# Optimization experiments

Hardware: AMD Instinct MI355X
Metric: run time of the kernel (lower is better)

The kernel has to match this reference:

```python
import jax, jax.numpy as jnp
import numpy as np

N_HEADS = 8
HEAD_SIZE = 64
CONTEXT = 256
D_MODEL = 512
MASK_NEG = 1e9


def setup_inputs() -> dict:
    key = jax.random.key(0)
    k1, k2, k3, k4 = jax.random.split(key, 4)
    B, T, D = 2, 4096, D_MODEL
    # Glorot-uniform-ish scales
    def glorot(k, shape):
        fan_in, fan_out = shape[-2], shape[-1]
        lim = jnp.sqrt(6.0 / (fan_in + fan_out))
        return jax.random.uniform(k, shape, jnp.float32, -lim, lim)
    inputs = jax.random.normal(k1, (B, T, D), dtype=jnp.float32)
    WQ = glorot(k2, (N_HEADS, D, HEAD_SIZE))
    WV = glorot(k3, (N_HEADS, D, HEAD_SIZE))
    WU = glorot(k4, (N_HEADS * HEAD_SIZE, D))
    return {"inputs": inputs, "WQ": WQ, "WV": WV, "WU": WU}


def reference(inputs, WQ, WV, WU):
    B, T, D = inputs.shape
    H, _, S = WQ.shape
    # Q, V: [B, H, T, hs]
    Q = jnp.einsum('btd,hds->bhts', inputs, WQ)
    V = jnp.einsum('btd,hds->bhts', inputs, WV)
    # Scores use Q @ V^T (no separate K in this module): [B, H, T, T]
    scores = jnp.einsum('bhts,bhus->bhtu', Q, V) / jnp.sqrt(jnp.float32(S))
    idx = jnp.arange(T)
    band = jnp.abs(idx[:, None] - idx[None, :]) <= CONTEXT  # [T, T] bool
    scores = scores - MASK_NEG * (~band).astype(scores.dtype)
    W = jax.nn.softmax(scores, axis=-1)
    C = jnp.einsum('bhtu,bhus->bhts', W, V)  # [B, H, T, hs]
    # concat heads along feature dim: [B, T, H*hs]
    C = C.transpose(0, 2, 1, 3).reshape(B, T, H * S)
    return C @ WU  # [B, T, D]
```

## Files before the change

kernel.cpp:

```cpp
#include <hip/hip_runtime.h>

#define TSEQ 4096
#define DM 512
#define NH 8
#define HS 64
#define CTX 256

typedef __attribute__((ext_vector_type(8))) short bf16x8;
typedef __attribute__((ext_vector_type(4))) float f32x4;
typedef unsigned short u16;
typedef unsigned long long ull;

__device__ __forceinline__ u16 f2bf(float x) {
    unsigned u = __float_as_uint(x);
    unsigned r = (u + 0x7fffu + ((u >> 16) & 1u)) >> 16;
    return (u16)r;
}
__device__ __forceinline__ float bf2f(u16 b) {
    return __uint_as_float(((unsigned)b) << 16);
}
__device__ __forceinline__ unsigned bf16dup(float p) {
    unsigned w;
    asm("v_cvt_pk_bf16_f32 %0, %1, %1" : "=v"(w) : "v"(p));
    return w;
}
template<int CTRL>
__device__ __forceinline__ float dpp_ror(float x) {
    int xi = __float_as_int(x);
    return __int_as_float(__builtin_amdgcn_update_dpp(xi, xi, CTRL, 0xf, 0xf, false));
}
__device__ __forceinline__ float row16_max(float v) {
    v = fmaxf(v, dpp_ror<0x121>(v));
    v = fmaxf(v, dpp_ror<0x122>(v));
    v = fmaxf(v, dpp_ror<0x124>(v));
    v = fmaxf(v, dpp_ror<0x128>(v));
    return v;
}

#define MFMA(a, b, c) __builtin_amdgcn_mfma_f32_16x16x32_bf16((a), (b), (c), 0, 0, 0)

__global__ __launch_bounds__(256) void presplit_x(
    const float* __restrict__ X, u16* __restrict__ Xh)
{
    size_t idx = ((size_t)blockIdx.x * 256 + threadIdx.x) * 8;
    float4 p0 = *(const float4*)(X + idx);
    float4 p1 = *(const float4*)(X + idx + 4);
    float v[8] = {p0.x, p0.y, p0.z, p0.w, p1.x, p1.y, p1.z, p1.w};
    bf16x8 h;
    #pragma unroll
    for (int i = 0; i < 8; ++i) h[i] = (short)f2bf(v[i]);
    *(bf16x8*)(Xh + idx) = h;
}

__global__ __launch_bounds__(256) void presplit_w(
    const float* __restrict__ WQ, const float* __restrict__ WV,
    const float* __restrict__ WU,
    u16* __restrict__ WQt_h, u16* __restrict__ WVt_h, u16* __restrict__ WUt_h)
{
    int gidx = blockIdx.x * 256 + threadIdx.x;
    int a = gidx >> 18;
    int r = gidx & 262143;
    float val;
    u16* dh;
    int dst;
    if (a < 2) {
        int h = r >> 15, s = (r >> 9) & 63, d = r & 511;
        const float* W = (a == 0) ? WQ : WV;
        val = W[h * 32768 + d * 64 + s];
        dst = h * 32768 + s * 512 + d;
        dh = (a == 0) ? WQt_h : WVt_h;
    } else {
        int n = r >> 9, k = r & 511;
        val = WU[k * 512 + n];
        dst = n * 512 + k;
        dh = WUt_h;
    }
    dh[dst] = f2bf(val);
}

__global__ __launch_bounds__(256) void gemm_mfma(
    const u16* __restrict__ Ah_g,
    const u16* __restrict__ B0h, const u16* __restrict__ B1h,
    u16* __restrict__ O0h,
    u16* __restrict__ O1h,
    u16* __restrict__ O1t,
    float* __restrict__ Of,
    int mode)
{
    __shared__ u16 Ah[128][64];
    __shared__ u16 Bh[64][64];

    const int tid = threadIdx.x;
    const int w = tid >> 6, lane = tid & 63;
    const int lg = lane >> 4, ln = lane & 15;
    const int r0 = blockIdx.x * 128;
    const int y = blockIdx.y;

    const u16* Bsh;
    if (mode == 0) {
        Bsh = ((y < 8) ? B0h + (size_t)y * 32768 : B1h + (size_t)(y - 8) * 32768);
    } else {
        Bsh = B0h + (size_t)y * 64 * 512;
    }

    const int r_a = tid >> 3;
    const int kc  = tid & 7;
    const int wcol = (kc * 8) ^ ((r_a & 7) << 3);
    const size_t gA = (size_t)(r0 + r_a) * DM + kc * 8;
    const size_t gB = (size_t)r_a * 512 + kc * 8;

    bf16x8 a0h, a1h, a2h, a3h, b0h, b1h;

    #define GLOAD(k0)                                                   \
        a0h = *(const bf16x8*)(Ah_g + gA + (k0));                       \
        a1h = *(const bf16x8*)(Ah_g + gA + 32 * DM + (k0));             \
        a2h = *(const bf16x8*)(Ah_g + gA + 64 * DM + (k0));             \
        a3h = *(const bf16x8*)(Ah_g + gA + 96 * DM + (k0));             \
        b0h = *(const bf16x8*)(Bsh + gB + (k0));                        \
        b1h = *(const bf16x8*)(Bsh + gB + 32 * 512 + (k0));

    f32x4 acc[2][4];
    #pragma unroll
    for (int i = 0; i < 2; ++i)
        #pragma unroll
        for (int j = 0; j < 4; ++j)
            acc[i][j] = (f32x4){0.f, 0.f, 0.f, 0.f};

    GLOAD(0);

    for (int kt = 0; kt < 8; ++kt) {
        __syncthreads();
        *(bf16x8*)&Ah[r_a][wcol]      = a0h;
        *(bf16x8*)&Ah[r_a + 32][wcol] = a1h;
        *(bf16x8*)&Ah[r_a + 64][wcol] = a2h;
        *(bf16x8*)&Ah[r_a + 96][wcol] = a3h;
        *(bf16x8*)&Bh[r_a][wcol]      = b0h;
        *(bf16x8*)&Bh[r_a + 32][wcol] = b1h;
        __syncthreads();
        if (kt < 7) { GLOAD((kt + 1) * 64); }

        #pragma unroll
        for (int kk = 0; kk < 2; ++kk) {
            const int fc = (kk * 32 + lg * 8) ^ ((ln & 7) << 3);
            bf16x8 ah[2], bh2[4];
            #pragma unroll
            for (int ti = 0; ti < 2; ++ti)
                ah[ti] = *(const bf16x8*)&Ah[w * 32 + ti * 16 + ln][fc];
            #pragma unroll
            for (int nj = 0; nj < 4; ++nj)
                bh2[nj] = *(const bf16x8*)&Bh[nj * 16 + ln][fc];
            #pragma unroll
            for (int ti = 0; ti < 2; ++ti)
                #pragma unroll
                for (int nj = 0; nj < 4; ++nj)
                    acc[ti][nj] = MFMA(ah[ti], bh2[nj], acc[ti][nj]);
        }
    }
    #undef GLOAD

    const float qscale = (mode == 0 && y < 8) ? 0.18033688f : 1.0f;
    #pragma unroll
    for (int ti = 0; ti < 2; ++ti)
        #pragma unroll
        for (int nj = 0; nj < 4; ++nj) {
            u16 hb[4];
            #pragma unroll
            for (int r = 0; r < 4; ++r) {
                float val = acc[ti][nj][r] * qscale;
                hb[r] = f2bf(val);
                int t = r0 + w * 32 + ti * 16 + lg * 4 + r;
                int n = nj * 16 + ln;
                if (mode == 0) {
                    int bh = (t >> 12) * NH + (y & 7);
                    size_t off = ((size_t)bh * TSEQ + (t & (TSEQ - 1))) * HS + n;
                    if (y < 8) O0h[off] = hb[r];
                    else       O1h[off] = hb[r];
                } else {
                    Of[(size_t)t * DM + y * 64 + n] = val;
                }
            }
            if (mode == 0 && y >= 8) {
                int t = r0 + w * 32 + ti * 16 + lg * 4;
                int n = nj * 16 + ln;
                int bh = (t >> 12) * NH + (y & 7);
                size_t off = (size_t)bh * TSEQ * HS + (size_t)n * TSEQ + (t & (TSEQ - 1));
                ull pk = (ull)hb[0] | ((ull)hb[1] << 16)
                       | ((ull)hb[2] << 32) | ((ull)hb[3] << 48);
                *(ull*)(O1t + off) = pk;
            }
        }
}

__global__ __launch_bounds__(256) void attn_v9(
    const u16* __restrict__ Qh_g,
    const u16* __restrict__ Vnh_g, const u16* __restrict__ Vth_g,
    u16* __restrict__ Ch)
{
    __shared__ u16 Vn_h[64][64];
    __shared__ u16 Vt_h[64][64];
    __shared__ unsigned Ps[4][16][32];

    const int tid = threadIdx.x;
    const int w = tid >> 6, lane = tid & 63;
    const int lg = lane >> 4, ln = lane & 15;
    const int raw = blockIdx.x;
    const int swz = (raw & 7) * 128 + (raw >> 3);
    const int ttile = swz & 63;
    const int bh = swz >> 6;
    const int t0 = ttile * 64;
    const size_t base = (size_t)bh * TSEQ * HS;
    const u16* Qph = Qh_g + base;
    const u16* Vph = Vnh_g + base;
    const u16* Vth = Vth_g + base;

    bf16x8 qh[2];
    #pragma unroll
    for (int kk = 0; kk < 2; ++kk) {
        size_t off = (size_t)(t0 + w * 16 + ln) * HS + kk * 32 + lg * 8;
        qh[kk] = *(const bf16x8*)(Qph + off);
    }

    bf16x8 ones_frag;
    #pragma unroll
    for (int e = 0; e < 8; ++e)
        ones_frag[e] = (ln == 0) ? (short)0x3F80 : (short)0;

    f32x4 o[4], o4;
    float m[4];
    #pragma unroll
    for (int j = 0; j < 4; ++j) {
        o[j] = (f32x4){0.f, 0.f, 0.f, 0.f};
        m[j] = -1e30f;
    }
    o4 = (f32x4){0.f, 0.f, 0.f, 0.f};

    int u_lo = t0 - CTX; if (u_lo < 0) u_lo = 0;
    int u_hi = t0 + 64 + CTX; if (u_hi > TSEQ) u_hi = TSEQ;

    const int sr = tid >> 3;
    const int c8 = (tid & 7) * 8;
    const int wcA = c8 ^ ((sr & 7) << 3);

    bf16x8 vn0h, vn1h, vt0h, vt1h;
    #define VL(u0v)                                                             \
        vn0h = *(const bf16x8*)(Vph + (size_t)((u0v) + sr) * HS + c8);          \
        vn1h = *(const bf16x8*)(Vph + (size_t)((u0v) + sr + 32) * HS + c8);     \
        vt0h = *(const bf16x8*)(Vth + (size_t)sr * TSEQ + (u0v) + c8);          \
        vt1h = *(const bf16x8*)(Vth + (size_t)(sr + 32) * TSEQ + (u0v) + c8);

    VL(u_lo);

    for (int u0 = u_lo; u0 < u_hi; u0 += 64) {
        __syncthreads();
        *(bf16x8*)&Vn_h[sr][wcA]      = vn0h;
        *(bf16x8*)&Vn_h[sr + 32][wcA] = vn1h;
        *(bf16x8*)&Vt_h[sr][wcA]      = vt0h;
        *(bf16x8*)&Vt_h[sr + 32][wcA] = vt1h;
        __syncthreads();
        if (u0 + 64 < u_hi) { VL(u0 + 64); }

        f32x4 s[4];
        #pragma unroll
        for (int j = 0; j < 4; ++j) s[j] = (f32x4){0.f, 0.f, 0.f, 0.f};

        #pragma unroll
        for (int kk = 0; kk < 2; ++kk) {
            const int fc = (kk * 32 + lg * 8) ^ ((ln & 7) << 3);
            bf16x8 vh[4];
            #pragma unroll
            for (int uj = 0; uj < 4; ++uj)
                vh[uj] = *(const bf16x8*)&Vn_h[uj * 16 + ln][fc];
            #pragma unroll
            for (int uj = 0; uj < 4; ++uj)
                s[uj] = MFMA(qh[kk], vh[uj], s[uj]);
        }

        bool needmask = ((t0 + 63 - u0) > CTX) || ((u0 + 63 - t0) > CTX);
        if (needmask) {
            #pragma unroll
            for (int uj = 0; uj < 4; ++uj)
                #pragma unroll
                for (int r = 0; r < 4; ++r) {
                    int t = t0 + w * 16 + lg * 4 + r;
                    int u = u0 + uj * 16 + ln;
                    int d = t - u; if (d < 0) d = -d;
                    if (d > CTX) s[uj][r] = -1e30f;
                }
        }

        float rm[4];
        bool need = false;
        #pragma unroll
        for (int r = 0; r < 4; ++r) {
            float v = fmaxf(fmaxf(s[0][r], s[1][r]), fmaxf(s[2][r], s[3][r]));
            rm[r] = row16_max(v);
            need |= (rm[r] > m[r] + 8.f);
        }
        if (__any(need)) {
            #pragma unroll
            for (int r = 0; r < 4; ++r) {
                float mn = fmaxf(m[r], rm[r]);
                float sc2 = exp2f(m[r] - mn);
                m[r] = mn;
                o4[r] *= sc2;
                #pragma unroll
                for (int sj = 0; sj < 4; ++sj)
                    o[sj][r] *= sc2;
            }
        }
        #pragma unroll
        for (int r = 0; r < 4; ++r)
            #pragma unroll
            for (int uj = 0; uj < 4; ++uj)
                s[uj][r] = exp2f(s[uj][r] - m[r]);

        #pragma unroll
        for (int kk = 0; kk < 2; ++kk) {
            #pragma unroll
            for (int u2 = 0; u2 < 2; ++u2) {
                int uj = kk * 2 + u2;
                #pragma unroll
                for (int r = 0; r < 4; ++r) {
                    int trow = lg * 4 + r;
                    int ucol = (u2 * 16 + ln) ^ ((trow & 7) << 2);
                    Ps[w][trow][ucol] = bf16dup(s[uj][r]);
                }
            }

            bf16x8 ph, vth4[4];
            {
                int sw = (ln & 7) << 2;
                uint4 q0 = *(const uint4*)&Ps[w][ln][(lg * 8) ^ sw];
                uint4 q1 = *(const uint4*)&Ps[w][ln][(lg * 8 + 4) ^ sw];
                union { unsigned u[4]; bf16x8 v; } H;
                H.u[0] = __builtin_amdgcn_perm(q0.y, q0.x, 0x05040100u);
                H.u[1] = __builtin_amdgcn_perm(q0.w, q0.z, 0x05040100u);
                H.u[2] = __builtin_amdgcn_perm(q1.y, q1.x, 0x05040100u);
                H.u[3] = __builtin_amdgcn_perm(q1.w, q1.z, 0x05040100u);
                ph = H.v;
            }
            const int fct = (kk * 32 + lg * 8) ^ ((ln & 7) << 3);
            #pragma unroll
            for (int sj = 0; sj < 4; ++sj)
                vth4[sj] = *(const bf16x8*)&Vt_h[sj * 16 + ln][fct];
            #pragma unroll
            for (int sj = 0; sj < 4; ++sj)
                o[sj] = MFMA(ph, vth4[sj], o[sj]);
            o4 = MFMA(ph, ones_frag, o4);
        }
    }
    #undef VL

    const int b = bh >> 3, h = bh & 7;
    #pragma unroll
    for (int r = 0; r < 4; ++r) {
        float ls = __shfl(o4[r], (lane >> 4) << 4);
        float inv = 1.f / ls;
        int t = t0 + w * 16 + lg * 4 + r;
        #pragma unroll
        for (int sj = 0; sj < 4; ++sj) {
            int ss = sj * 16 + ln;
            float val = o[sj][r] * inv;
            size_t off = ((size_t)(b * TSEQ + t)) * DM + h * HS + ss;
            Ch[off] = f2bf(val);
        }
    }
}

extern "C" void kernel_launch(void* const* d_in, const int* in_sizes, int n_in,
                              void* d_out, int out_size, void* d_ws, size_t ws_size,
                              hipStream_t stream) {
    const float* X  = (const float*)d_in[0];
    const float* WQ = (const float*)d_in[1];
    const float* WV = (const float*)d_in[2];
    const float* WU = (const float*)d_in[3];
    float* out = (float*)d_out;

    const size_t SZ = 8388608;
    char* ws = (char*)d_ws;

    u16* Xh = (u16*)(ws);
    u16* Qh = (u16*)(ws + 2 * SZ);
    u16* Vh = (u16*)(ws + 4 * SZ);
    u16* Vth = (u16*)(ws + 6 * SZ);
    char* wsw = ws + 8 * SZ;
    u16* WQt_h = (u16*)(wsw);
    u16* WVt_h = (u16*)(wsw + 524288);
    u16* WUt_h = (u16*)(wsw + 2 * 524288);

    presplit_x<<<2048, 256, 0, stream>>>(X, Xh);
    presplit_w<<<3072, 256, 0, stream>>>(WQ, WV, WU, WQt_h, WVt_h, WUt_h);
    gemm_mfma<<<dim3(64, 16), 256, 0, stream>>>(
        Xh, WQt_h, WVt_h, Qh, Vh, Vth, nullptr, 0);
    attn_v9<<<1024, 256, 0, stream>>>(Qh, Vh, Vth, Xh);
    gemm_mfma<<<dim3(64, 8), 256, 0, stream>>>(
        Xh, WUt_h, nullptr, nullptr, nullptr, nullptr, out, 1);
}
```

Measured before the change: 78.22 us.

## Process 128-key chunks in attention and split output GEMM into smaller tiles

The attention kernel now stages 128 keys per shared-memory load instead of 64 and processes two 64-key halves per barrier pair, which cuts synchronisation and load-loop overhead. The output projection gets a dedicated kernel with 64-row tiles and twice as many blocks, for better occupancy of the GPU. The cost is more shared memory and registers per attention block, which may lower occupancy.

```diff
diff --git a/kernel.cpp b/kernel.cpp
--- a/kernel.cpp
+++ b/kernel.cpp
@@ -78,14 +78,12 @@
     dh[dst] = f2bf(val);
 }
 
-__global__ __launch_bounds__(256) void gemm_mfma(
+__global__ __launch_bounds__(256) void gemm_qv(
     const u16* __restrict__ Ah_g,
     const u16* __restrict__ B0h, const u16* __restrict__ B1h,
     u16* __restrict__ O0h,
     u16* __restrict__ O1h,
-    u16* __restrict__ O1t,
-    float* __restrict__ Of,
-    int mode)
+    u16* __restrict__ O1t)
 {
     __shared__ u16 Ah[128][64];
     __shared__ u16 Bh[64][64];
@@ -96,12 +94,8 @@
     const int r0 = blockIdx.x * 128;
     const int y = blockIdx.y;
 
-    const u16* Bsh;
-    if (mode == 0) {
-        Bsh = ((y < 8) ? B0h + (size_t)y * 32768 : B1h + (size_t)(y - 8) * 32768);
-    } else {
-        Bsh = B0h + (size_t)y * 64 * 512;
-    }
+    const u16* Bsh = (y < 8) ? B0h + (size_t)y * 32768
+                             : B1h + (size_t)(y - 8) * 32768;
 
     const int r_a = tid >> 3;
     const int kc  = tid & 7;
@@ -158,7 +152,7 @@
     }
     #undef GLOAD
 
-    const float qscale = (mode == 0 && y < 8) ? 0.18033688f : 1.0f;
+    const float qscale = (y < 8) ? 0.18033688f : 1.0f;
     #pragma unroll
     for (int ti = 0; ti < 2; ++ti)
         #pragma unroll
@@ -170,16 +164,12 @@
                 hb[r] = f2bf(val);
                 int t = r0 + w * 32 + ti * 16 + lg * 4 + r;
                 int n = nj * 16 + ln;
-                if (mode == 0) {
-                    int bh = (t >> 12) * NH + (y & 7);
-                    size_t off = ((size_t)bh * TSEQ + (t & (TSEQ - 1))) * HS + n;
-                    if (y < 8) O0h[off] = hb[r];
-                    else       O1h[off] = hb[r];
-                } else {
-                    Of[(size_t)t * DM + y * 64 + n] = val;
-                }
-            }
-            if (mode == 0 && y >= 8) {
+                int bh = (t >> 12) * NH + (y & 7);
+                size_t off = ((size_t)bh * TSEQ + (t & (TSEQ - 1))) * HS + n;
+                if (y < 8) O0h[off] = hb[r];
+                else       O1h[off] = hb[r];
+            }
+            if (y >= 8) {
                 int t = r0 + w * 32 + ti * 16 + lg * 4;
                 int n = nj * 16 + ln;
                 int bh = (t >> 12) * NH + (y & 7);
@@ -191,13 +181,82 @@
         }
 }
 
-__global__ __launch_bounds__(256) void attn_v9(
+__global__ __launch_bounds__(256) void gemm_out(
+    const u16* __restrict__ Ah_g, const u16* __restrict__ Bt_h,
+    float* __restrict__ Of)
+{
+    __shared__ u16 Ah[64][64];
+    __shared__ u16 Bh[64][64];
+
+    const int tid = threadIdx.x;
+    const int w = tid >> 6, lane = tid & 63;
+    const int lg = lane >> 4, ln = lane & 15;
+    const int r0 = blockIdx.x * 64;
+    const int y = blockIdx.y;
+
+    const u16* Bsh = Bt_h + (size_t)y * 64 * 512;
+
+    const int r_a = tid >> 3;
+    const int kc  = tid & 7;
+    const int wcol = (kc * 8) ^ ((r_a & 7) << 3);
+    const size_t gA = (size_t)(r0 + r_a) * DM + kc * 8;
+    const size_t gB = (size_t)r_a * 512 + kc * 8;
+
+    bf16x8 a0h, a1h, b0h, b1h;
+
+    #define GLOAD(k0)                                                   \
+        a0h = *(const bf16x8*)(Ah_g + gA + (k0));                       \
+        a1h = *(const bf16x8*)(Ah_g + gA + 32 * DM + (k0));             \
+        b0h = *(const bf16x8*)(Bsh + gB + (k0));                        \
+        b1h = *(const bf16x8*)(Bsh + gB + 32 * 512 + (k0));
+
+    f32x4 acc[4];
+    #pragma unroll
+    for (int j = 0; j < 4; ++j)
+        acc[j] = (f32x4){0.f, 0.f, 0.f, 0.f};
+
+    GLOAD(0);
+
+    for (int kt = 0; kt < 8; ++kt) {
+        __syncthreads();
+        *(bf16x8*)&Ah[r_a][wcol]      = a0h;
+        *(bf16x8*)&Ah[r_a + 32][wcol] = a1h;
+        *(bf16x8*)&Bh[r_a][wcol]      = b0h;
+        *(bf16x8*)&Bh[r_a + 32][wcol] = b1h;
+        __syncthreads();
+        if (kt < 7) { GLOAD((kt + 1) * 64); }
+
+        #pragma unroll
+        for (int kk = 0; kk < 2; ++kk) {
+            const int fc = (kk * 32 + lg * 8) ^ ((ln & 7) << 3);
+            bf16x8 ah = *(const bf16x8*)&Ah[w * 16 + ln][fc];
+            bf16x8 bh2[4];
+            #pragma unroll
+            for (int nj = 0; nj < 4; ++nj)
+                bh2[nj] = *(const bf16x8*)&Bh[nj * 16 + ln][fc];
+            #pragma unroll
+            for (int nj = 0; nj < 4; ++nj)
+                acc[nj] = MFMA(ah, bh2[nj], acc[nj]);
+        }
+    }
+    #undef GLOAD
+
+    #pragma unroll
+    for (int nj = 0; nj < 4; ++nj)
+        #pragma unroll
+        for (int r = 0; r < 4; ++r) {
+            int t = r0 + w * 16 + lg * 4 + r;
+            Of[(size_t)t * DM + y * 64 + nj * 16 + ln] = acc[nj][r];
+        }
+}
+
+__global__ __launch_bounds__(256) void attn_v10(
     const u16* __restrict__ Qh_g,
     const u16* __restrict__ Vnh_g, const u16* __restrict__ Vth_g,
     u16* __restrict__ Ch)
 {
-    __shared__ u16 Vn_h[64][64];
-    __shared__ u16 Vt_h[64][64];
+    __shared__ u16 Vn_h[128][64];
+    __shared__ u16 Vt_h[64][128];
     __shared__ unsigned Ps[4][16][32];
 
     const int tid = threadIdx.x;
@@ -241,112 +300,126 @@
     const int c8 = (tid & 7) * 8;
     const int wcA = c8 ^ ((sr & 7) << 3);
 
-    bf16x8 vn0h, vn1h, vt0h, vt1h;
+    bf16x8 vn0, vn1, vn2, vn3, vt00, vt01, vt10, vt11;
     #define VL(u0v)                                                             \
-        vn0h = *(const bf16x8*)(Vph + (size_t)((u0v) + sr) * HS + c8);          \
-        vn1h = *(const bf16x8*)(Vph + (size_t)((u0v) + sr + 32) * HS + c8);     \
-        vt0h = *(const bf16x8*)(Vth + (size_t)sr * TSEQ + (u0v) + c8);          \
-        vt1h = *(const bf16x8*)(Vth + (size_t)(sr + 32) * TSEQ + (u0v) + c8);
+        vn0 = *(const bf16x8*)(Vph + (size_t)((u0v) + sr) * HS + c8);           \
+        vn1 = *(const bf16x8*)(Vph + (size_t)((u0v) + sr + 32) * HS + c8);      \
+        vn2 = *(const bf16x8*)(Vph + (size_t)((u0v) + sr + 64) * HS + c8);      \
+        vn3 = *(const bf16x8*)(Vph + (size_t)((u0v) + sr + 96) * HS + c8);      \
+        vt00 = *(const bf16x8*)(Vth + (size_t)sr * TSEQ + (u0v) + c8);          \
+        vt01 = *(const bf16x8*)(Vth + (size_t)sr * TSEQ + (u0v) + 64 + c8);     \
+        vt10 = *(const bf16x8*)(Vth + (size_t)(sr + 32) * TSEQ + (u0v) + c8);   \
+        vt11 = *(const bf16x8*)(Vth + (size_t)(sr + 32) * TSEQ + (u0v) + 64 + c8);
 
     VL(u_lo);
 
-    for (int u0 = u_lo; u0 < u_hi; u0 += 64) {
-        __syncthreads();
-        *(bf16x8*)&Vn_h[sr][wcA]      = vn0h;
-        *(bf16x8*)&Vn_h[sr + 32][wcA] = vn1h;
-        *(bf16x8*)&Vt_h[sr][wcA]      = vt0h;
-        *(bf16x8*)&Vt_h[sr + 32][wcA] = vt1h;
-        __syncthreads();
-        if (u0 + 64 < u_hi) { VL(u0 + 64); }
-
-        f32x4 s[4];
-        #pragma unroll
-        for (int j = 0; j < 4; ++j) s[j] = (f32x4){0.f, 0.f, 0.f, 0.f};
-
-        #pragma unroll
-        for (int kk = 0; kk < 2; ++kk) {
-            const int fc = (kk * 32 + lg * 8) ^ ((ln & 7) << 3);
-            bf16x8 vh[4];
-            #pragma unroll
-            for (int uj = 0; uj < 4; ++uj)
-                vh[uj] = *(const bf16x8*)&Vn_h[uj * 16 + ln][fc];
-            #pragma unroll
-            for (int uj = 0; uj < 4; ++uj)
-                s[uj] = MFMA(qh[kk], vh[uj], s[uj]);
-        }
-
-        bool needmask = ((t0 + 63 - u0) > CTX) || ((u0 + 63 - t0) > CTX);
-        if (needmask) {
-            #pragma unroll
-            for (int uj = 0; uj < 4; ++uj)
+    for (int u0 = u_lo; u0 < u_hi; u0 += 128) {
+        __syncthreads();
+        *(bf16x8*)&Vn_h[sr][wcA]       = vn0;
+        *(bf16x8*)&Vn_h[sr + 32][wcA]  = vn1;
+        *(bf16x8*)&Vn_h[sr + 64][wcA]  = vn2;
+        *(bf16x8*)&Vn_h[sr + 96][wcA]  = vn3;
+        *(bf16x8*)&Vt_h[sr][wcA]       = vt00;
+        *(bf16x8*)&Vt_h[sr][64 + wcA]  = vt01;
+        *(bf16x8*)&Vt_h[sr + 32][wcA]      = vt10;
+        *(bf16x8*)&Vt_h[sr + 32][64 + wcA] = vt11;
+        __syncthreads();
+        if (u0 + 128 < u_hi) { VL(u0 + 128); }
+
+        #pragma unroll
+        for (int half = 0; half < 2; ++half) {
+            int uc = u0 + half * 64;
+            if (uc >= u_hi) break;
+
+            f32x4 s[4];
+            #pragma unroll
+            for (int j = 0; j < 4; ++j) s[j] = (f32x4){0.f, 0.f, 0.f, 0.f};
+
+            #pragma unroll
+            for (int kk = 0; kk < 2; ++kk) {
+                const int fc = (kk * 32 + lg * 8) ^ ((ln & 7) << 3);
+                bf16x8 vh[4];
+                #pragma unroll
+                for (int uj = 0; uj < 4; ++uj)
+                    vh[uj] = *(const bf16x8*)&Vn_h[half * 64 + uj * 16 + ln][fc];
+                #pragma unroll
+                for (int uj = 0; uj < 4; ++uj)
+                    s[uj] = MFMA(qh[kk], vh[uj], s[uj]);
+            }
+
+            bool needmask = ((t0 + 63 - uc) > CTX) || ((uc + 63 - t0) > CTX);
+            if (needmask) {
+                #pragma unroll
+                for (int uj = 0; uj < 4; ++uj)
+                    #pragma unroll
+                    for (int r = 0; r < 4; ++r) {
+                        int t = t0 + w * 16 + lg * 4 + r;
+                        int u = uc + uj * 16 + ln;
+                        int d = t - u; if (d < 0) d = -d;
+                        if (d > CTX) s[uj][r] = -1e30f;
+                    }
+            }
+
+            float rm[4];
+            bool need = false;
+            #pragma unroll
+            for (int r = 0; r < 4; ++r) {
+                float v = fmaxf(fmaxf(s[0][r], s[1][r]), fmaxf(s[2][r], s[3][r]));
+                rm[r] = row16_max(v);
+                need |= (rm[r] > m[r] + 8.f);
+            }
+            if (__any(need)) {
                 #pragma unroll
                 for (int r = 0; r < 4; ++r) {
-                    int t = t0 + w * 16 + lg * 4 + r;
-                    int u = u0 + uj * 16 + ln;
-                    int d = t - u; if (d < 0) d = -d;
-                    if (d > CTX) s[uj][r] = -1e30f;
+                    float mn = fmaxf(m[r], rm[r]);
+                    float sc2 = exp2f(m[r] - mn);
+                    m[r] = mn;
+                    o4[r] *= sc2;
+                    #pragma unroll
+                    for (int sj = 0; sj < 4; ++sj)
+                        o[sj][r] *= sc2;
                 }
-        }
-
-        float rm[4];
-        bool need = false;
-        #pragma unroll
-        for (int r = 0; r < 4; ++r) {
-            float v = fmaxf(fmaxf(s[0][r], s[1][r]), fmaxf(s[2][r], s[3][r]));
-            rm[r] = row16_max(v);
-            need |= (rm[r] > m[r] + 8.f);
-        }
-        if (__any(need)) {
-            #pragma unroll
-            for (int r = 0; r < 4; ++r) {
-                float mn = fmaxf(m[r], rm[r]);
-                float sc2 = exp2f(m[r] - mn);
-                m[r] = mn;
-                o4[r] *= sc2;
+            }
+            #pragma unroll
+            for (int r = 0; r < 4; ++r)
+                #pragma unroll
+                for (int uj = 0; uj < 4; ++uj)
+                    s[uj][r] = exp2f(s[uj][r] - m[r]);
+
+            #pragma unroll
+            for (int kk = 0; kk < 2; ++kk) {
+                #pragma unroll
+                for (int u2 = 0; u2 < 2; ++u2) {
+                    int uj = kk * 2 + u2;
+                    #pragma unroll
+                    for (int r = 0; r < 4; ++r) {
+                        int trow = lg * 4 + r;
+                        int ucol = (u2 * 16 + ln) ^ ((trow & 7) << 2);
+                        Ps[w][trow][ucol] = bf16dup(s[uj][r]);
+                    }
+                }
+
+                bf16x8 ph, vth4[4];
+                {
+                    int sw = (ln & 7) << 2;
+                    uint4 q0 = *(const uint4*)&Ps[w][ln][(lg * 8) ^ sw];
+                    uint4 q1 = *(const uint4*)&Ps[w][ln][(lg * 8 + 4) ^ sw];
+                    union { unsigned u[4]; bf16x8 v; } H;
+                    H.u[0] = __builtin_amdgcn_perm(q0.y, q0.x, 0x05040100u);
+                    H.u[1] = __builtin_amdgcn_perm(q0.w, q0.z, 0x05040100u);
+                    H.u[2] = __builtin_amdgcn_perm(q1.y, q1.x, 0x05040100u);
+                    H.u[3] = __builtin_amdgcn_perm(q1.w, q1.z, 0x05040100u);
+                    ph = H.v;
+                }
+                const int fct = (kk * 32 + lg * 8) ^ ((ln & 7) << 3);
                 #pragma unroll
                 for (int sj = 0; sj < 4; ++sj)
-                    o[sj][r] *= sc2;
-            }
-        }
-        #pragma unroll
-        for (int r = 0; r < 4; ++r)
-            #pragma unroll
-            for (int uj = 0; uj < 4; ++uj)
-                s[uj][r] = exp2f(s[uj][r] - m[r]);
-
-        #pragma unroll
-        for (int kk = 0; kk < 2; ++kk) {
-            #pragma unroll
-            for (int u2 = 0; u2 < 2; ++u2) {
-                int uj = kk * 2 + u2;
-                #pragma unroll
-                for (int r = 0; r < 4; ++r) {
-                    int trow = lg * 4 + r;
-                    int ucol = (u2 * 16 + ln) ^ ((trow & 7) << 2);
-                    Ps[w][trow][ucol] = bf16dup(s[uj][r]);
-                }
-            }
-
-            bf16x8 ph, vth4[4];
-            {
-                int sw = (ln & 7) << 2;
-                uint4 q0 = *(const uint4*)&Ps[w][ln][(lg * 8) ^ sw];
-                uint4 q1 = *(const uint4*)&Ps[w][ln][(lg * 8 + 4) ^ sw];
-                union { unsigned u[4]; bf16x8 v; } H;
-                H.u[0] = __builtin_amdgcn_perm(q0.y, q0.x, 0x05040100u);
-                H.u[1] = __builtin_amdgcn_perm(q0.w, q0.z, 0x05040100u);
-                H.u[2] = __builtin_amdgcn_perm(q1.y, q1.x, 0x05040100u);
-                H.u[3] = __builtin_amdgcn_perm(q1.w, q1.z, 0x05040100u);
-                ph = H.v;
-            }
-            const int fct = (kk * 32 + lg * 8) ^ ((ln & 7) << 3);
-            #pragma unroll
-            for (int sj = 0; sj < 4; ++sj)
-                vth4[sj] = *(const bf16x8*)&Vt_h[sj * 16 + ln][fct];
-            #pragma unroll
-            for (int sj = 0; sj < 4; ++sj)
-                o[sj] = MFMA(ph, vth4[sj], o[sj]);
-            o4 = MFMA(ph, ones_frag, o4);
+                    vth4[sj] = *(const bf16x8*)&Vt_h[sj * 16 + ln][half * 64 + fct];
+                #pragma unroll
+                for (int sj = 0; sj < 4; ++sj)
+                    o[sj] = MFMA(ph, vth4[sj], o[sj]);
+                o4 = MFMA(ph, ones_frag, o4);
+            }
         }
     }
     #undef VL
@@ -390,9 +463,7 @@
 
     presplit_x<<<2048, 256, 0, stream>>>(X, Xh);
     presplit_w<<<3072, 256, 0, stream>>>(WQ, WV, WU, WQt_h, WVt_h, WUt_h);
-    gemm_mfma<<<dim3(64, 16), 256, 0, stream>>>(
-        Xh, WQt_h, WVt_h, Qh, Vh, Vth, nullptr, 0);
-    attn_v9<<<1024, 256, 0, stream>>>(Qh, Vh, Vth, Xh);
-    gemm_mfma<<<dim3(64, 8), 256, 0, stream>>>(
-        Xh, WUt_h, nullptr, nullptr, nullptr, nullptr, out, 1);
-}
+    gemm_qv<<<dim3(64, 16), 256, 0, stream>>>(Xh, WQt_h, WVt_h, Qh, Vh, Vth);
+    attn_v10<<<1024, 256, 0, stream>>>(Qh, Vh, Vth, Xh);
+    gemm_out<<<dim3(128, 8), 256, 0, stream>>>(Xh, WUt_h, out);
+}
```

After: 79.45 us. No clear change (+1.6%).
